# Performance work log

Measured on AMD Instinct MI355X. Metric: run time of the kernel, lower is better.

Reference implementation:

```python
import jax, jax.numpy as jnp
import numpy as np

B, N, D = 4, 16384, 128       # batch, tokens (mesh points), input_dim
H, DH = 8, 64                 # heads, dim_head
INNER = H * DH


def setup_inputs() -> dict:
    key = jax.random.key(0)
    ks = jax.random.split(key, 7)
    s = 0.02  # weight init scale
    return {
        "queries": jax.random.normal(ks[0], (B, N, D), jnp.float32),
        "keys":    jax.random.normal(ks[1], (B, N, D), jnp.float32),
        "values":  jax.random.normal(ks[2], (B, N, D), jnp.float32),
        "Wq": jax.random.normal(ks[3], (INNER, D), jnp.float32) * s,
        "Wk": jax.random.normal(ks[4], (INNER, D), jnp.float32) * s,
        "Wo": jax.random.normal(ks[5], (D, INNER), jnp.float32) * s,
        "bo": jnp.zeros((D,), jnp.float32),
    }


def _split_heads(x, b, n):
    # [b, n, h*d] -> [b, h, n, d]
    return x.reshape(b, n, H, DH).transpose(0, 2, 1, 3)


def reference(queries, keys, values, Wq, Wk, Wo, bo):
    b, n, _ = queries.shape
    q = _split_heads(queries @ Wq.T, b, n)
    k = _split_heads(keys    @ Wk.T, b, n)
    # NOTE: original source applies to_k to values (bug kept for faithfulness)
    v = _split_heads(values  @ Wk.T, b, n)
    # Galerkin linear attention, associative order: q @ (k^T v) / n.
    # (In the runnable no-mask path the instance norms are computed but
    #  discarded by the original code, so they are omitted here.)
    dots = jnp.einsum('bhnd,bhne->bhde', k, v)          # [b,h,d,d]
    out = jnp.einsum('bhnd,bhde->bhne', q, dots) / n    # [b,h,n,d]
    out = out.transpose(0, 2, 1, 3).reshape(b, n, INNER)
    return out @ Wo.T + bo
```

## Files before the change

### kernel.cpp

```cpp
#include <hip/hip_runtime.h>
#include <hip/hip_bf16.h>

#define BB    4
#define NN    16384
#define DD    128
#define HH    8
#define DHH   64
#define INNER 512
#define PC    128

typedef __attribute__((ext_vector_type(8))) short bf16x8;
typedef __attribute__((ext_vector_type(4))) short short4_t;
typedef __attribute__((ext_vector_type(4))) float f32x4;
typedef unsigned short ushort_t;

#define MFMA(a, b, c) __builtin_amdgcn_mfma_f32_16x16x32_bf16((a), (b), (c), 0, 0, 0)

__device__ __forceinline__ short f2bf(float x) {
    union { float f; unsigned u; } v; v.f = x;
    unsigned u = v.u;
    u += 0x7fffu + ((u >> 16) & 1u);
    return (short)(u >> 16);
}

__device__ __forceinline__ float bf2f(ushort_t us) {
    union { unsigned u; float f; } v;
    v.u = ((unsigned)us) << 16;
    return v.f;
}

__device__ __forceinline__ bf16x8 load_row8(const float* __restrict__ p) {
    f32x4 a = *(const f32x4*)p;
    f32x4 b = *(const f32x4*)(p + 4);
    bf16x8 r;
    r[0] = f2bf(a[0]); r[1] = f2bf(a[1]); r[2] = f2bf(a[2]); r[3] = f2bf(a[3]);
    r[4] = f2bf(b[0]); r[5] = f2bf(b[1]); r[6] = f2bf(b[2]); r[7] = f2bf(b[3]);
    return r;
}

__device__ __forceinline__ bf16x8 load_col8(const float* __restrict__ p, int stride) {
    bf16x8 r;
#pragma unroll
    for (int j = 0; j < 8; ++j) r[j] = f2bf(p[(size_t)j * stride]);
    return r;
}

__global__ __launch_bounds__(512, 4) void k1_partialS_ab(
        const float* __restrict__ keys, const float* __restrict__ vals,
        const float* __restrict__ Wq, const float* __restrict__ Wk,
        const float* __restrict__ Wo,
        ushort_t* __restrict__ partial, ushort_t* __restrict__ Abf,
        ushort_t* __restrict__ BTbf, float* __restrict__ G) {
    const int lane = threadIdx.x & 63;
    const int w    = threadIdx.x >> 6;
    const int ml   = lane & 15;
    const int quad = lane >> 4;

    __shared__ short tK[2][32][132];
    __shared__ short tV[2][32][132];

    if (blockIdx.x < BB * PC) {
        const int b     = blockIdx.x >> 7;
        const int chunk = blockIdx.x & (PC - 1);
        const int r0    = chunk * (NN / PC);
        const int mw    = w & 3;
        const int nw    = w >> 2;

        const float* kbase = keys + (size_t)b * NN * DD;
        const float* vbase = vals + (size_t)b * NN * DD;

        const int lin0 = (int)threadIdx.x;
        const int ca0  = (2 * mw + 0) * 16 + ml;
        const int ca1  = (2 * mw + 1) * 16 + ml;

        f32x4 acc[2][4];
#pragma unroll
        for (int i = 0; i < 2; ++i)
#pragma unroll
            for (int t = 0; t < 4; ++t) acc[i][t] = (f32x4){0.f, 0.f, 0.f, 0.f};

        {
            const float* kp = kbase + (size_t)r0 * DD;
            const float* vp = vbase + (size_t)r0 * DD;
#pragma unroll
            for (int it = 0; it < 2; ++it) {
                const int lin = lin0 + it * 512;
                const int row = lin >> 5;
                const int c4  = (lin & 31) << 2;
                f32x4 kk = *(const f32x4*)(kp + (size_t)row * DD + c4);
                f32x4 vv = *(const f32x4*)(vp + (size_t)row * DD + c4);
                short4_t ks, vs;
#pragma unroll
                for (int j = 0; j < 4; ++j) { ks[j] = f2bf(kk[j]); vs[j] = f2bf(vv[j]); }
                *(short4_t*)&tK[0][row][c4] = ks;
                *(short4_t*)&tV[0][row][c4] = vs;
            }
        }
        __syncthreads();

        for (int s = 0; s < 4; ++s) {
            const int cur   = s & 1;
            const bool more = (s < 3);

            f32x4 kreg[2], vreg[2];
            if (more) {
                const float* kp = kbase + (size_t)(r0 + (s + 1) * 32) * DD;
                const float* vp = vbase + (size_t)(r0 + (s + 1) * 32) * DD;
#pragma unroll
                for (int it = 0; it < 2; ++it) {
                    const int lin = lin0 + it * 512;
                    const int row = lin >> 5;
                    const int c4  = (lin & 31) << 2;
                    kreg[it] = *(const f32x4*)(kp + (size_t)row * DD + c4);
                    vreg[it] = *(const f32x4*)(vp + (size_t)row * DD + c4);
                }
            }

            {
                bf16x8 a0, a1;
#pragma unroll
                for (int j = 0; j < 8; ++j) {
                    a0[j] = tK[cur][quad * 8 + j][ca0];
                    a1[j] = tK[cur][quad * 8 + j][ca1];
                }
#pragma unroll
                for (int t = 0; t < 4; ++t) {
                    const int cb = (nw * 4 + t) * 16 + ml;
                    bf16x8 bf;
#pragma unroll
                    for (int j = 0; j < 8; ++j) bf[j] = tV[cur][quad * 8 + j][cb];
                    acc[0][t] = MFMA(a0, bf, acc[0][t]);
                    acc[1][t] = MFMA(a1, bf, acc[1][t]);
                }
            }

            if (more) {
                __syncthreads();
                const int nb = cur ^ 1;
#pragma unroll
                for (int it = 0; it < 2; ++it) {
                    const int lin = lin0 + it * 512;
                    const int row = lin >> 5;
                    const int c4  = (lin & 31) << 2;
                    short4_t ks, vs;
#pragma unroll
                    for (int j = 0; j < 4; ++j) {
                        ks[j] = f2bf(kreg[it][j]);
                        vs[j] = f2bf(vreg[it][j]);
                    }
                    *(short4_t*)&tK[nb][row][c4] = ks;
                    *(short4_t*)&tV[nb][row][c4] = vs;
                }
                __syncthreads();
            }
        }

        ushort_t* outp = partial + (size_t)blockIdx.x * DD * DD;
#pragma unroll
        for (int i = 0; i < 2; ++i) {
            const int mrow = (2 * mw + i) * 16 + quad * 4;
#pragma unroll
            for (int t = 0; t < 4; ++t) {
                const int col = (nw * 4 + t) * 16 + ml;
#pragma unroll
                for (int r = 0; r < 4; ++r)
                    outp[(size_t)(mrow + r) * DD + col] = (ushort_t)f2bf(acc[i][t][r]);
            }
        }
    } else {
        const int ab    = blockIdx.x - BB * PC;
        const int h     = ab & 7;
        const int which = ab >> 3;
        const float* Wkh = Wk + (size_t)h * DHH * DD;

        {
            const int base = (ab * 512 + (int)threadIdx.x) * 8;
            *(f32x4*)&G[base]     = (f32x4){0.f, 0.f, 0.f, 0.f};
            *(f32x4*)&G[base + 4] = (f32x4){0.f, 0.f, 0.f, 0.f};
        }

        f32x4 acc[8];
#pragma unroll
        for (int t = 0; t < 8; ++t) acc[t] = (f32x4){0.f, 0.f, 0.f, 0.f};

        if (which == 0) {
            const float* Wqh = Wq + (size_t)h * DHH * DD;
#pragma unroll
            for (int kc = 0; kc < 2; ++kc) {
                const int d0 = kc * 32 + quad * 8;
                bf16x8 a = load_col8(Wqh + (size_t)d0 * DD + w * 16 + ml, DD);
#pragma unroll
                for (int t = 0; t < 8; ++t) {
                    bf16x8 bf = load_col8(Wkh + (size_t)d0 * DD + t * 16 + ml, DD);
                    acc[t] = MFMA(a, bf, acc[t]);
                }
            }
            ushort_t* dst = Abf + (size_t)h * DD * DD;
#pragma unroll
            for (int t = 0; t < 8; ++t)
#pragma unroll
                for (int r = 0; r < 4; ++r)
                    dst[(size_t)(w * 16 + quad * 4 + r) * DD + t * 16 + ml] =
                        (ushort_t)f2bf(acc[t][r]);
        } else {
#pragma unroll
            for (int kc = 0; kc < 2; ++kc) {
                const int e0 = kc * 32 + quad * 8;
                bf16x8 a = load_row8(Wo + (size_t)(w * 16 + ml) * INNER + h * DHH + e0);
#pragma unroll
                for (int t = 0; t < 8; ++t) {
                    bf16x8 bf = load_col8(Wkh + (size_t)e0 * DD + t * 16 + ml, DD);
                    acc[t] = MFMA(a, bf, acc[t]);
                }
            }
            ushort_t* dst = BTbf + (size_t)h * DD * DD;
#pragma unroll
            for (int t = 0; t < 8; ++t)
#pragma unroll
                for (int r = 0; r < 4; ++r)
                    dst[(size_t)(w * 16 + quad * 4 + r) * DD + t * 16 + ml] =
                        (ushort_t)f2bf(acc[t][r]);
        }
    }
}

__global__ __launch_bounds__(128) void k2_reduce(
        const ushort_t* __restrict__ partial, ushort_t* __restrict__ SbfT) {
    const int tid = blockIdx.x * 128 + threadIdx.x;
    const int e   = tid * 2;
    const int b   = e >> 14;
    const int idx = e & 16383;
    const unsigned* p32 =
        (const unsigned*)(partial + ((size_t)b * PC) * DD * DD + idx);
    float s0 = 0.f, s1 = 0.f;
#pragma unroll 16
    for (int c = 0; c < PC; ++c) {
        const unsigned u = p32[(size_t)c * (DD * DD / 2)];
        s0 += bf2f((ushort_t)(u & 0xffffu));
        s1 += bf2f((ushort_t)(u >> 16));
    }
    const int c  = idx >> 7;
    const int cp = idx & 127;
    ushort_t* st = SbfT + (size_t)b * DD * DD;
    st[(size_t)(cp    ) * DD + c] = (ushort_t)f2bf(s0);
    st[(size_t)(cp + 1) * DD + c] = (ushort_t)f2bf(s1);
}

__global__ __launch_bounds__(512) void k3_middle(
        const ushort_t* __restrict__ SbfT, const ushort_t* __restrict__ Abf,
        const ushort_t* __restrict__ BTbf, float* __restrict__ G) {
    const int bi = blockIdx.x;
    const int b  = bi >> 6;
    const int h  = (bi >> 3) & 7;
    const int m0 = (bi & 7) * 16;
    const int lane = threadIdx.x & 63;
    const int w    = threadIdx.x >> 6;
    const int ml   = lane & 15;
    const int quad = lane >> 4;

    __shared__ short T[16 * 136];

    const ushort_t* Sb = SbfT + (size_t)b * DD * DD;
    const ushort_t* Ah = Abf  + (size_t)h * DD * DD;
    const ushort_t* Bh = BTbf + (size_t)h * DD * DD;

    {
        f32x4 acc = (f32x4){0.f, 0.f, 0.f, 0.f};
#pragma unroll
        for (int kc = 0; kc < 4; ++kc) {
            const int c0 = kc * 32 + quad * 8;
            bf16x8 a  = *(const bf16x8*)&Ah[(size_t)(m0 + ml) * DD + c0];
            bf16x8 bf = *(const bf16x8*)&Sb[(size_t)(w * 16 + ml) * DD + c0];
            acc = MFMA(a, bf, acc);
        }
#pragma unroll
        for (int r = 0; r < 4; ++r)
            T[(quad * 4 + r) * 136 + w * 16 + ml] = f2bf(acc[r]);
    }
    __syncthreads();

    {
        f32x4 acc = (f32x4){0.f, 0.f, 0.f, 0.f};
#pragma unroll
        for (int kc = 0; kc < 4; ++kc) {
            const int k0 = kc * 32 + quad * 8;
            bf16x8 a  = *(const bf16x8*)&T[ml * 136 + k0];
            bf16x8 bf = *(const bf16x8*)&Bh[(size_t)(w * 16 + ml) * DD + k0];
            acc = MFMA(a, bf, acc);
        }
        float* Gb = G + (size_t)b * DD * DD;
#pragma unroll
        for (int r = 0; r < 4; ++r)
            atomicAdd(&Gb[(m0 + quad * 4 + r) * DD + w * 16 + ml], acc[r]);
    }
}

__global__ __launch_bounds__(512, 4) void k4_final(
        const float* __restrict__ queries, const float* __restrict__ G,
        const float* __restrict__ bo, float* __restrict__ outp) {
    const int b  = blockIdx.x >> 7;
    const int r0 = (blockIdx.x & 127) * 128;

    __shared__ short Gt[128 * 136];
    {
        const float* Gb = G + (size_t)b * DD * DD;
        const float invN = 6.103515625e-05f;
#pragma unroll 4
        for (int it = 0; it < 32; ++it) {
            const int idx = (int)threadIdx.x + it * 512;
            const int cp = idx >> 7, c = idx & 127;
            Gt[c * 136 + cp] = f2bf(Gb[idx] * invN);
        }
    }
    __syncthreads();

    const int lane = threadIdx.x & 63;
    const int w    = threadIdx.x >> 6;
    const int ml   = lane & 15;
    const int quad = lane >> 4;
    const float* qbase = queries + ((size_t)b * NN + r0) * DD;

    f32x4 acc[8];
#pragma unroll
    for (int t = 0; t < 8; ++t) acc[t] = (f32x4){0.f, 0.f, 0.f, 0.f};

#pragma unroll
    for (int kc = 0; kc < 4; ++kc) {
        const int k0 = kc * 32 + quad * 8;
        bf16x8 a = load_row8(qbase + (size_t)(w * 16 + ml) * DD + k0);
#pragma unroll
        for (int t = 0; t < 8; ++t) {
            bf16x8 bf = *(const bf16x8*)&Gt[(t * 16 + ml) * 136 + k0];
            acc[t] = MFMA(a, bf, acc[t]);
        }
    }

    float* ob = outp + ((size_t)b * NN + r0) * DD;
#pragma unroll
    for (int t = 0; t < 8; ++t) {
        const int c = t * 16 + ml;
        const float boc = bo[c];
#pragma unroll
        for (int r = 0; r < 4; ++r)
            ob[(size_t)(w * 16 + quad * 4 + r) * DD + c] = acc[t][r] + boc;
    }
}

extern "C" void kernel_launch(void* const* d_in, const int* in_sizes, int n_in,
                              void* d_out, int out_size, void* d_ws, size_t ws_size,
                              hipStream_t stream) {
    const float* queries = (const float*)d_in[0];
    const float* keys    = (const float*)d_in[1];
    const float* values  = (const float*)d_in[2];
    const float* Wq      = (const float*)d_in[3];
    const float* Wk      = (const float*)d_in[4];
    const float* Wo      = (const float*)d_in[5];
    const float* bo      = (const float*)d_in[6];
    float* out = (float*)d_out;

    ushort_t* SbfT = (ushort_t*)d_ws;
    float* G = (float*)d_ws + (size_t)BB * DD * DD;
    ushort_t* Abf     = (ushort_t*)(G + (size_t)BB * DD * DD);
    ushort_t* BTbf    = Abf  + (size_t)HH * DD * DD;
    ushort_t* partial = BTbf + (size_t)HH * DD * DD;

    hipLaunchKernelGGL(k1_partialS_ab, dim3(BB * PC + 16), dim3(512), 0, stream,
                       keys, values, Wq, Wk, Wo, partial, Abf, BTbf, G);
    hipLaunchKernelGGL(k2_reduce, dim3(256), dim3(128), 0, stream,
                       partial, SbfT);
    hipLaunchKernelGGL(k3_middle, dim3(256), dim3(512), 0, stream,
                       SbfT, Abf, BTbf, G);
    hipLaunchKernelGGL(k4_final, dim3(512), dim3(512), 0, stream,
                       queries, G, bo, out);
}
```

Measured before the change: 159.9 us.

## Deepen K/V prefetch to two stages and schedule weight blocks first

Unrolls the four-stage partial-S loop into an explicit schedule that keeps two stages of global K/V loads in flight in registers, using raw s_barrier with lgkmcnt waits and sched_barrier fences in place of __syncthreads. It also reorders the block indexing so the 16 weight-preparation blocks get the lowest block IDs and launch first. The aim is to hide global memory latency better in this bandwidth-bound reduction, at the cost of more live registers, which may reduce occupancy.

```diff
diff --git a/kernel.cpp b/kernel.cpp
--- a/kernel.cpp
+++ b/kernel.cpp
@@ -15,6 +15,10 @@
 typedef unsigned short ushort_t;
 
 #define MFMA(a, b, c) __builtin_amdgcn_mfma_f32_16x16x32_bf16((a), (b), (c), 0, 0, 0)
+
+#define ASM_LGKM0() asm volatile("s_waitcnt lgkmcnt(0)" ::: "memory")
+#define FENCE()     __builtin_amdgcn_sched_barrier(0)
+#define BAR()       __builtin_amdgcn_s_barrier()
 
 __device__ __forceinline__ short f2bf(float x) {
     union { float f; unsigned u; } v; v.f = x;
@@ -59,9 +63,10 @@
     __shared__ short tK[2][32][132];
     __shared__ short tV[2][32][132];
 
-    if (blockIdx.x < BB * PC) {
-        const int b     = blockIdx.x >> 7;
-        const int chunk = blockIdx.x & (PC - 1);
+    if (blockIdx.x >= 16) {
+        const int mb    = blockIdx.x - 16;
+        const int b     = mb >> 7;
+        const int chunk = mb & (PC - 1);
         const int r0    = chunk * (NN / PC);
         const int mw    = w & 3;
         const int nw    = w >> 2;
@@ -73,89 +78,84 @@
         const int ca0  = (2 * mw + 0) * 16 + ml;
         const int ca1  = (2 * mw + 1) * 16 + ml;
 
+        const int row0 = lin0 >> 5,          row1 = (lin0 + 512) >> 5;
+        const int c40  = (lin0 & 31) << 2,   c41  = ((lin0 + 512) & 31) << 2;
+
         f32x4 acc[2][4];
 #pragma unroll
         for (int i = 0; i < 2; ++i)
 #pragma unroll
             for (int t = 0; t < 4; ++t) acc[i][t] = (f32x4){0.f, 0.f, 0.f, 0.f};
 
-        {
-            const float* kp = kbase + (size_t)r0 * DD;
-            const float* vp = vbase + (size_t)r0 * DD;
+        f32x4 kpre[2][2], vpre[2][2];
+
+        auto issueL = [&](int sidx, int slot) {
+            const float* kp = kbase + (size_t)(r0 + sidx * 32) * DD;
+            const float* vp = vbase + (size_t)(r0 + sidx * 32) * DD;
+            kpre[slot][0] = *(const f32x4*)(kp + (size_t)row0 * DD + c40);
+            vpre[slot][0] = *(const f32x4*)(vp + (size_t)row0 * DD + c40);
+            kpre[slot][1] = *(const f32x4*)(kp + (size_t)row1 * DD + c41);
+            vpre[slot][1] = *(const f32x4*)(vp + (size_t)row1 * DD + c41);
+        };
+
+        auto wstage = [&](int slot, int nb) {
 #pragma unroll
             for (int it = 0; it < 2; ++it) {
-                const int lin = lin0 + it * 512;
-                const int row = lin >> 5;
-                const int c4  = (lin & 31) << 2;
-                f32x4 kk = *(const f32x4*)(kp + (size_t)row * DD + c4);
-                f32x4 vv = *(const f32x4*)(vp + (size_t)row * DD + c4);
+                const int row = it ? row1 : row0;
+                const int c4  = it ? c41  : c40;
                 short4_t ks, vs;
 #pragma unroll
-                for (int j = 0; j < 4; ++j) { ks[j] = f2bf(kk[j]); vs[j] = f2bf(vv[j]); }
-                *(short4_t*)&tK[0][row][c4] = ks;
-                *(short4_t*)&tV[0][row][c4] = vs;
-            }
-        }
-        __syncthreads();
-
-        for (int s = 0; s < 4; ++s) {
-            const int cur   = s & 1;
-            const bool more = (s < 3);
-
-            f32x4 kreg[2], vreg[2];
-            if (more) {
-                const float* kp = kbase + (size_t)(r0 + (s + 1) * 32) * DD;
-                const float* vp = vbase + (size_t)(r0 + (s + 1) * 32) * DD;
-#pragma unroll
-                for (int it = 0; it < 2; ++it) {
-                    const int lin = lin0 + it * 512;
-                    const int row = lin >> 5;
-                    const int c4  = (lin & 31) << 2;
-                    kreg[it] = *(const f32x4*)(kp + (size_t)row * DD + c4);
-                    vreg[it] = *(const f32x4*)(vp + (size_t)row * DD + c4);
+                for (int j = 0; j < 4; ++j) {
+                    ks[j] = f2bf(kpre[slot][it][j]);
+                    vs[j] = f2bf(vpre[slot][it][j]);
                 }
-            }
-
-            {
-                bf16x8 a0, a1;
-#pragma unroll
-                for (int j = 0; j < 8; ++j) {
-                    a0[j] = tK[cur][quad * 8 + j][ca0];
-                    a1[j] = tK[cur][quad * 8 + j][ca1];
-                }
-#pragma unroll
-                for (int t = 0; t < 4; ++t) {
-                    const int cb = (nw * 4 + t) * 16 + ml;
-                    bf16x8 bf;
-#pragma unroll
-                    for (int j = 0; j < 8; ++j) bf[j] = tV[cur][quad * 8 + j][cb];
-                    acc[0][t] = MFMA(a0, bf, acc[0][t]);
-                    acc[1][t] = MFMA(a1, bf, acc[1][t]);
-                }
-            }
-
-            if (more) {
-                __syncthreads();
-                const int nb = cur ^ 1;
-#pragma unroll
-                for (int it = 0; it < 2; ++it) {
-                    const int lin = lin0 + it * 512;
-                    const int row = lin >> 5;
-                    const int c4  = (lin & 31) << 2;
-                    short4_t ks, vs;
-#pragma unroll
-                    for (int j = 0; j < 4; ++j) {
-                        ks[j] = f2bf(kreg[it][j]);
-                        vs[j] = f2bf(vreg[it][j]);
-                    }
-                    *(short4_t*)&tK[nb][row][c4] = ks;
-                    *(short4_t*)&tV[nb][row][c4] = vs;
-                }
-                __syncthreads();
-            }
-        }
-
-        ushort_t* outp = partial + (size_t)blockIdx.x * DD * DD;
+                *(short4_t*)&tK[nb][row][c4] = ks;
+                *(short4_t*)&tV[nb][row][c4] = vs;
+            }
+        };
+
+        auto compute = [&](int cur) {
+            bf16x8 a0, a1;
+#pragma unroll
+            for (int j = 0; j < 8; ++j) {
+                a0[j] = tK[cur][quad * 8 + j][ca0];
+                a1[j] = tK[cur][quad * 8 + j][ca1];
+            }
+#pragma unroll
+            for (int t = 0; t < 4; ++t) {
+                const int cb = (nw * 4 + t) * 16 + ml;
+                bf16x8 bf;
+#pragma unroll
+                for (int j = 0; j < 8; ++j) bf[j] = tV[cur][quad * 8 + j][cb];
+                acc[0][t] = MFMA(a0, bf, acc[0][t]);
+                acc[1][t] = MFMA(a1, bf, acc[1][t]);
+            }
+        };
+
+        issueL(0, 0); issueL(1, 1);
+        wstage(0, 0);
+        ASM_LGKM0(); FENCE(); BAR();
+
+        issueL(2, 0);
+        compute(0);
+        ASM_LGKM0(); FENCE(); BAR();
+        wstage(1, 1);
+        ASM_LGKM0(); FENCE(); BAR();
+
+        issueL(3, 1);
+        compute(1);
+        ASM_LGKM0(); FENCE(); BAR();
+        wstage(0, 0);
+        ASM_LGKM0(); FENCE(); BAR();
+
+        compute(0);
+        ASM_LGKM0(); FENCE(); BAR();
+        wstage(1, 1);
+        ASM_LGKM0(); FENCE(); BAR();
+
+        compute(1);
+
+        ushort_t* outp = partial + (size_t)mb * DD * DD;
 #pragma unroll
         for (int i = 0; i < 2; ++i) {
             const int mrow = (2 * mw + i) * 16 + quad * 4;
@@ -168,7 +168,7 @@
             }
         }
     } else {
-        const int ab    = blockIdx.x - BB * PC;
+        const int ab    = blockIdx.x;
         const int h     = ab & 7;
         const int which = ab >> 3;
         const float* Wkh = Wk + (size_t)h * DHH * DD;
```

Measured after the change: 161.5 us. Within noise of the previous version (+1.0%).
